# Kernel optimization log

Hardware: AMD Instinct MI355X
Metric: run time of the kernel (lower is better)

The kernel has to match this reference:

```python
import jax, jax.numpy as jnp
import numpy as np

HIDDEN = 1024
HEADS = 16
HEAD_DIM = HIDDEN // HEADS
EPS = 1e-5


def setup_inputs() -> dict:
    key = jax.random.key(0)
    ks = jax.random.split(key, 9)
    B, S, H = 2, 2048, HIDDEN
    scale = 1.0 / np.sqrt(H)
    inp = {
        "hidden_states": jax.random.normal(ks[0], (B, S, H), dtype=jnp.float32),
        "Wq": jax.random.normal(ks[1], (H, H), dtype=jnp.float32) * scale,
        "bq": jnp.zeros((H,), jnp.float32),
        "Wk": jax.random.normal(ks[2], (H, H), dtype=jnp.float32) * scale,
        "bk": jnp.zeros((H,), jnp.float32),
        "Wv": jax.random.normal(ks[3], (H, H), dtype=jnp.float32) * scale,
        "bv": jnp.zeros((H,), jnp.float32),
        "Wo": jax.random.normal(ks[4], (H, H), dtype=jnp.float32) * scale,
        "bo": jnp.zeros((H,), jnp.float32),
        "gamma": jnp.ones((H,), jnp.float32),
        "beta": jnp.zeros((H,), jnp.float32),
    }
    return inp


def reference(hidden_states, Wq, bq, Wk, bk, Wv, bv, Wo, bo, gamma, beta):
    B, S, H = hidden_states.shape
    residual = hidden_states

    def shape(x):  # [B,S,H] -> [B,heads,S,head_dim]
        return x.reshape(B, S, HEADS, HEAD_DIM).transpose(0, 2, 1, 3)

    q = shape(hidden_states @ Wq + bq)
    k = shape(hidden_states @ Wk + bk)
    v = shape(hidden_states @ Wv + bv)

    scores = jnp.einsum("bhqd,bhkd->bhqk", q, k) / jnp.sqrt(
        jnp.asarray(HEAD_DIM, hidden_states.dtype))
    probs = jax.nn.softmax(scores, axis=-1)
    context = jnp.einsum("bhqk,bhkd->bhqd", probs, v)
    context = context.transpose(0, 2, 1, 3).reshape(B, S, H)

    output = context @ Wo + bo
    x = output + residual
    mu = jnp.mean(x, axis=-1, keepdims=True)
    var = jnp.mean(jnp.square(x - mu), axis=-1, keepdims=True)
    return (x - mu) * jax.lax.rsqrt(var + EPS) * gamma + beta
```

## Files before the change

kernel.cpp:

```cpp
#include <hip/hip_runtime.h>
#include <hip/hip_bf16.h>
#include <math.h>

#define HIDDEN 1024
#define HEADS 16
#define HEAD_DIM 64
#define EPS 1e-5f

typedef __attribute__((ext_vector_type(8))) short bf16x8;
typedef __attribute__((ext_vector_type(4))) float f32x4;

#if defined(__has_builtin)
#if __has_builtin(__builtin_amdgcn_exp2f)
#define EXP2(x) __builtin_amdgcn_exp2f(x)
#endif
#endif
#ifndef EXP2
#define EXP2(x) exp2f(x)
#endif

#define QSCALE 0.18033688011112042f

__device__ __forceinline__ short f2bf(float f) {
    union { float f; unsigned u; } v; v.f = f;
    unsigned r = v.u + 0x7fffu + ((v.u >> 16) & 1u);
    return (short)(r >> 16);
}

__device__ __forceinline__ void gl_lds16(const void* g, void* l) {
    __builtin_amdgcn_global_load_lds(
        (const __attribute__((address_space(1))) void*)g,
        (__attribute__((address_space(3))) void*)l, 16, 0, 0);
}

__global__ __launch_bounds__(256) void cast_bf16_kernel(
    const float* __restrict__ in, short* __restrict__ out, int n)
{
    int i = (blockIdx.x * 256 + threadIdx.x) * 4;
    if (i >= n) return;
    float4 v = *(const float4*)(in + i);
    short o[4] = { f2bf(v.x), f2bf(v.y), f2bf(v.z), f2bf(v.w) };
    *(uint2*)(out + i) = *(uint2*)o;
}

__global__ __launch_bounds__(256) void wtrans_kernel(
    const float* __restrict__ Wq, const float* __restrict__ Wk,
    const float* __restrict__ Wv, const float* __restrict__ Wo,
    short* __restrict__ Wt3, short* __restrict__ Wot)
{
    const int wsel = blockIdx.z;
    const float* W = (wsel == 0) ? Wq : (wsel == 1) ? Wk : (wsel == 2) ? Wv : Wo;
    short* dst = (wsel < 3) ? (Wt3 + (size_t)wsel * 1024 * 1024) : Wot;
    const float scale = (wsel == 0) ? QSCALE : 1.0f;

    __shared__ short tile[32][33];
    int n0 = blockIdx.x * 32;
    int k0 = blockIdx.y * 32;
    int tx = threadIdx.x & 31;
    int ty = threadIdx.x >> 5;
    #pragma unroll
    for (int i = 0; i < 32; i += 8)
        tile[ty + i][tx] = f2bf(W[(size_t)(k0 + ty + i) * 1024 + n0 + tx] * scale);
    __syncthreads();
    #pragma unroll
    for (int i = 0; i < 32; i += 8)
        dst[(size_t)(n0 + ty + i) * 1024 + k0 + tx] = tile[tx][ty + i];
}

__global__ __launch_bounds__(256) void concat_bias_kernel(
    const float* __restrict__ bq, const float* __restrict__ bk,
    const float* __restrict__ bv, float* __restrict__ b3)
{
    int i = blockIdx.x * 256 + threadIdx.x;
    if (i >= 3072) return;
    float v = (i < 1024) ? bq[i] * QSCALE
            : (i < 2048) ? bk[i - 1024] : bv[i - 2048];
    b3[i] = v;
}

__global__ __launch_bounds__(256) void gemm_bt_mfma(
    const short* __restrict__ A, const short* __restrict__ Bt,
    const float* __restrict__ bias,
    void* __restrict__ C0, int ldc0,
    void* __restrict__ C1, int split_col, int ldc1,
    const float* __restrict__ resid,
    int M, int N, int K, int out_bf16)
{
    __shared__ short As[128 * 32];
    __shared__ short Bs[128 * 32];
    const int tid = threadIdx.x;
    const int wave = tid >> 6, lane = tid & 63;
    const int ln16 = lane & 15, quad = lane >> 4;
    const int wm = (wave >> 1) * 64, wn = (wave & 1) * 64;
    const int brow = blockIdx.y * 128, bcol = blockIdx.x * 128;

    const int sr  = lane >> 2;
    const int scb = lane & 3;

    f32x4 acc[4][4];
    #pragma unroll
    for (int mt = 0; mt < 4; ++mt)
        #pragma unroll
        for (int nt = 0; nt < 4; ++nt) acc[mt][nt] = (f32x4){0.f, 0.f, 0.f, 0.f};

    for (int k0 = 0; k0 < K; k0 += 32) {
        __syncthreads();
        #pragma unroll
        for (int i = 0; i < 2; ++i) {
            int rb = i * 64 + wave * 16;
            int r  = rb + sr;
            int csrc = (scb ^ ((r >> 1) & 3)) * 8;
            gl_lds16(A  + (size_t)(brow + r) * K + k0 + csrc, &As[rb * 32]);
            gl_lds16(Bt + (size_t)(bcol + r) * K + k0 + csrc, &Bs[rb * 32]);
        }
        __syncthreads();

        bf16x8 af[4], bf[4];
        #pragma unroll
        for (int mt = 0; mt < 4; ++mt) {
            int r = wm + mt * 16 + ln16;
            af[mt] = *(const bf16x8*)&As[r * 32 + ((quad ^ ((r >> 1) & 3)) * 8)];
        }
        #pragma unroll
        for (int nt = 0; nt < 4; ++nt) {
            int r = wn + nt * 16 + ln16;
            bf[nt] = *(const bf16x8*)&Bs[r * 32 + ((quad ^ ((r >> 1) & 3)) * 8)];
        }
        #pragma unroll
        for (int mt = 0; mt < 4; ++mt)
            #pragma unroll
            for (int nt = 0; nt < 4; ++nt)
                acc[mt][nt] = __builtin_amdgcn_mfma_f32_16x16x32_bf16(
                    af[mt], bf[nt], acc[mt][nt], 0, 0, 0);
    }

    void* Cp = C0; int ld = ldc0; int coff = 0;
    if (bcol >= split_col) { Cp = C1; ld = ldc1; coff = split_col; }

    #pragma unroll
    for (int mt = 0; mt < 4; ++mt) {
        #pragma unroll
        for (int r = 0; r < 4; ++r) {
            int row = brow + wm + mt * 16 + quad * 4 + r;
            #pragma unroll
            for (int nt = 0; nt < 4; ++nt) {
                int col = bcol + wn + nt * 16 + ln16;
                float v = acc[mt][nt][r] + bias[col];
                if (resid) v += resid[(size_t)row * N + col];
                if (out_bf16) ((short*)Cp)[(size_t)row * ld + (col - coff)] = f2bf(v);
                else          ((float*)Cp)[(size_t)row * ld + (col - coff)] = v;
            }
        }
    }
}

__global__ __launch_bounds__(256) void vtranspose_kernel(
    const short* __restrict__ Vb, short* __restrict__ VT)
{
    __shared__ short t[64][72];
    const int c0 = blockIdx.x * 64;
    const int r0 = blockIdx.y * 64;
    const int tid = threadIdx.x;
    #pragma unroll
    for (int i = 0; i < 2; ++i) {
        int idx = tid + i * 256;
        int r = idx >> 3, cc = (idx & 7) * 8;
        *(uint4*)&t[r][cc] = *(const uint4*)(Vb + (size_t)(r0 + r) * 1024 + c0 + cc);
    }
    __syncthreads();
    #pragma unroll
    for (int i = 0; i < 2; ++i) {
        int idx = tid + i * 256;
        int c = idx >> 3, rr = (idx & 7) * 8;
        short tmp[8];
        #pragma unroll
        for (int j = 0; j < 8; ++j) tmp[j] = t[rr + j][c];
        *(uint4*)(VT + (size_t)(c0 + c) * 4096 + r0 + rr) = *(uint4*)tmp;
    }
}

__global__ __launch_bounds__(256, 2) void attn_mfma_kernel(
    const short* __restrict__ QKb, const short* __restrict__ VT,
    short* __restrict__ Ctx)
{
    const int S = 2048;
    const int h = blockIdx.x, qt = blockIdx.y, b = blockIdx.z;
    const int tid = threadIdx.x;
    const int wave = tid >> 6, lane = tid & 63;
    const int ln16 = lane & 15, quad = lane >> 4;

    __shared__ alignas(16) char smem[81920];
    char* Pw = smem + 65536 + wave * 4096;

    bf16x8 qf[4][2];
    #pragma unroll
    for (int qg = 0; qg < 4; ++qg)
        #pragma unroll
        for (int kb = 0; kb < 2; ++kb)
            qf[qg][kb] = *(const bf16x8*)(QKb +
                (size_t)(b * S + qt * 64 + qg * 16 + ln16) * 2048 +
                h * 64 + kb * 32 + quad * 8);

    bf16x8 ones;
    #pragma unroll
    for (int j = 0; j < 8; ++j) ones[j] = (short)0x3F80;

    f32x4 of[4][4], lacc[4];
    #pragma unroll
    for (int qg = 0; qg < 4; ++qg) {
        lacc[qg] = (f32x4){0.f, 0.f, 0.f, 0.f};
        #pragma unroll
        for (int nt = 0; nt < 4; ++nt) of[qg][nt] = (f32x4){0.f, 0.f, 0.f, 0.f};
    }

    auto stage = [&](int p, int kt) {
        short* ksb = (short*)(smem + p * 16384);
        short* vsb = (short*)(smem + 32768 + p * 16384);
        const int kr  = lane >> 3;
        const int kb8 = lane & 7;
        const int vr  = lane >> 4;
        const int vb16 = lane & 15;
        #pragma unroll
        for (int i = 0; i < 4; ++i) {
            int r = wave * 32 + i * 8 + kr;
            int ksrc = (kb8 ^ (r & 7)) * 8;
            gl_lds16(QKb + (size_t)(b * S + kt * 128 + r) * 2048 + 1024 + h * 64 + ksrc,
                     ksb + (wave * 32 + i * 8) * 64);
            int d = wave * 16 + i * 4 + vr;
            int vsrc = (vb16 ^ (d & 15)) * 8;
            gl_lds16(VT + (size_t)(h * 64 + d) * 4096 + b * S + kt * 128 + vsrc,
                     vsb + (wave * 16 + i * 4) * 128);
        }
    };

    stage(0, 0);

    for (int kt = 0; kt < 16; ++kt) {
        const int p = kt & 1;

        if (kt + 1 < 16) {
            stage(p ^ 1, kt + 1);
            asm volatile("s_waitcnt vmcnt(8)" ::: "memory");
        } else {
            asm volatile("s_waitcnt vmcnt(0)" ::: "memory");
        }
        __builtin_amdgcn_s_barrier();
        __builtin_amdgcn_sched_barrier(0);

        const short* ks = (const short*)(smem + p * 16384);
        const short* vs = (const short*)(smem + 32768 + p * 16384);
        const int t0w = wave * 32;

        #pragma unroll
        for (int kblk = 0; kblk < 2; ++kblk) {
            int rloc = t0w + kblk * 16 + ln16;
            bf16x8 kf0 = *(const bf16x8*)&ks[rloc * 64 + ((quad ^ (rloc & 7)) * 8)];
            bf16x8 kf1 = *(const bf16x8*)&ks[rloc * 64 + (((4 + quad) ^ (rloc & 7)) * 8)];
            #pragma unroll
            for (int qg = 0; qg < 4; ++qg) {
                f32x4 a = (f32x4){0.f, 0.f, 0.f, 0.f};
                a = __builtin_amdgcn_mfma_f32_16x16x32_bf16(kf0, qf[qg][0], a, 0, 0, 0);
                a = __builtin_amdgcn_mfma_f32_16x16x32_bf16(kf1, qf[qg][1], a, 0, 0, 0);
                float p0 = EXP2(a[0]), p1 = EXP2(a[1]);
                float p2 = EXP2(a[2]), p3 = EXP2(a[3]);
                union { __hip_bfloat162 h2; unsigned u; } c01, c23;
                c01.h2 = __float22bfloat162_rn(make_float2(p0, p1));
                c23.h2 = __float22bfloat162_rn(make_float2(p2, p3));
                uint2 w; w.x = c01.u; w.y = c23.u;
                int qrow = qg * 16 + ln16;
                int key = (qrow >> 1) & 3;
                int bblk = (kblk * 2 + (quad >> 1)) ^ key;
                *(uint2*)(Pw + qrow * 64 + bblk * 16 + (quad & 1) * 8) = w;
            }
        }

        bf16x8 pf[4];
        #pragma unroll
        for (int qg = 0; qg < 4; ++qg) {
            int qrow = qg * 16 + ln16;
            int key = (qrow >> 1) & 3;
            pf[qg] = *(const bf16x8*)(Pw + qrow * 64 + ((quad ^ key) * 16));
            lacc[qg] = __builtin_amdgcn_mfma_f32_16x16x32_bf16(pf[qg], ones, lacc[qg], 0, 0, 0);
        }
        #pragma unroll
        for (int nt = 0; nt < 4; ++nt) {
            int d = nt * 16 + ln16;
            bf16x8 vf = *(const bf16x8*)&vs[d * 128 + (((wave * 4 + quad) ^ (d & 15)) * 8)];
            #pragma unroll
            for (int qg = 0; qg < 4; ++qg)
                of[qg][nt] = __builtin_amdgcn_mfma_f32_16x16x32_bf16(pf[qg], vf, of[qg][nt], 0, 0, 0);
        }

        __builtin_amdgcn_sched_barrier(0);
        __builtin_amdgcn_s_barrier();
    }

    __syncthreads();

    float* Rw = (float*)(smem + wave * 4864);
    float* Lb = (float*)(smem + 4 * 4864);

    if (ln16 == 0) {
        #pragma unroll
        for (int qg = 0; qg < 4; ++qg)
            #pragma unroll
            for (int r = 0; r < 4; ++r)
                Lb[wave * 64 + qg * 16 + quad * 4 + r] = lacc[qg][r];
    }

    const int rq  = tid >> 2;
    const int rd0 = (tid & 3) * 4;
    float inv = 0.f;

    #pragma unroll
    for (int nt = 0; nt < 4; ++nt) {
        #pragma unroll
        for (int qg = 0; qg < 4; ++qg)
            #pragma unroll
            for (int r = 0; r < 4; ++r)
                Rw[(qg * 16 + quad * 4 + r) * 19 + ln16] = of[qg][nt][r];
        __syncthreads();
        if (nt == 0) {
            float l = Lb[rq] + Lb[64 + rq] + Lb[128 + rq] + Lb[192 + rq];
            inv = 1.f / l;
        }
        short o4[4];
        #pragma unroll
        for (int j = 0; j < 4; ++j) {
            int d = rd0 + j;
            float s = 0.f;
            #pragma unroll
            for (int w = 0; w < 4; ++w)
                s += ((const float*)(smem + w * 4864))[rq * 19 + d];
            o4[j] = f2bf(s * inv);
        }
        *(uint2*)(Ctx + (size_t)(b * S + qt * 64 + rq) * 1024 + h * 64 + nt * 16 + rd0) =
            *(uint2*)o4;
        __syncthreads();
    }
}

__global__ __launch_bounds__(256) void resln_kernel(
    const float* __restrict__ xin, const float* __restrict__ gamma,
    const float* __restrict__ beta, float* __restrict__ out)
{
    const int row = blockIdx.x;
    const int tid = threadIdx.x;
    const int wid = tid >> 6, lane = tid & 63;
    __shared__ float red[8];

    float4 x = *(const float4*)(xin + (size_t)row * HIDDEN + tid * 4);
    float s = x.x + x.y + x.z + x.w;
    #pragma unroll
    for (int off = 32; off > 0; off >>= 1) s += __shfl_xor(s, off, 64);
    if (lane == 0) red[wid] = s;
    __syncthreads();
    float mu = (red[0] + red[1] + red[2] + red[3]) * (1.f / HIDDEN);

    float dx = x.x - mu, dy = x.y - mu, dz = x.z - mu, dw = x.w - mu;
    float v = dx * dx + dy * dy + dz * dz + dw * dw;
    #pragma unroll
    for (int off = 32; off > 0; off >>= 1) v += __shfl_xor(v, off, 64);
    if (lane == 0) red[4 + wid] = v;
    __syncthreads();
    float var = (red[4] + red[5] + red[6] + red[7]) * (1.f / HIDDEN);
    float rstd = rsqrtf(var + EPS);

    float4 g = *(const float4*)(gamma + tid * 4);
    float4 bt = *(const float4*)(beta + tid * 4);
    float4 o;
    o.x = dx * rstd * g.x + bt.x;
    o.y = dy * rstd * g.y + bt.y;
    o.z = dz * rstd * g.z + bt.z;
    o.w = dw * rstd * g.w + bt.w;
    *(float4*)(out + (size_t)row * HIDDEN + tid * 4) = o;
}

extern "C" void kernel_launch(void* const* d_in, const int* in_sizes, int n_in,
                              void* d_out, int out_size, void* d_ws, size_t ws_size,
                              hipStream_t stream)
{
    const float* X     = (const float*)d_in[0];
    const float* Wq    = (const float*)d_in[1];
    const float* bq    = (const float*)d_in[2];
    const float* Wk    = (const float*)d_in[3];
    const float* bk    = (const float*)d_in[4];
    const float* Wv    = (const float*)d_in[5];
    const float* bv    = (const float*)d_in[6];
    const float* Wo    = (const float*)d_in[7];
    const float* bo    = (const float*)d_in[8];
    const float* gamma = (const float*)d_in[9];
    const float* beta  = (const float*)d_in[10];
    float* out = (float*)d_out;

    const int B = 2, S = 2048;
    const int M = B * S;
    const size_t mat = (size_t)M * HIDDEN;

    char* ws = (char*)d_ws;
    short* Xb  = (short*)(ws);
    short* VT  = (short*)(ws);
    short* Wot = (short*)(ws + (8ull << 20));
    short* Wt3 = (short*)(ws + (10ull << 20));
    float* b3  = (float*)(ws + (16ull << 20));
    short* QKb = (short*)(ws + (17ull << 20));
    float* Pj  = (float*)(ws + (17ull << 20));
    short* Vb  = (short*)(ws + (33ull << 20));
    short* Ctx = (short*)(ws + (33ull << 20));

    dim3 blk(256);

    cast_bf16_kernel<<<dim3((int)(mat / 4 / 256)), blk, 0, stream>>>(X, Xb, (int)mat);
    wtrans_kernel<<<dim3(32, 32, 4), blk, 0, stream>>>(Wq, Wk, Wv, Wo, Wt3, Wot);
    concat_bias_kernel<<<12, blk, 0, stream>>>(bq, bk, bv, b3);

    dim3 qkvgrid(3072 / 128, M / 128);
    gemm_bt_mfma<<<qkvgrid, blk, 0, stream>>>(Xb, Wt3, b3,
                                              QKb, 2048, Vb, 2048, 1024,
                                              nullptr, M, 3072, HIDDEN, 1);

    vtranspose_kernel<<<dim3(16, 64), blk, 0, stream>>>(Vb, VT);

    dim3 agrid(HEADS, S / 64, B);
    attn_mfma_kernel<<<agrid, blk, 0, stream>>>(QKb, VT, Ctx);

    dim3 ogrid(HIDDEN / 128, M / 128);
    gemm_bt_mfma<<<ogrid, blk, 0, stream>>>(Ctx, Wot, bo,
                                            Pj, 1024, nullptr, 1 << 30, 0,
                                            X, M, HIDDEN, HIDDEN, 0);

    resln_kernel<<<M, blk, 0, stream>>>(Pj, gamma, beta, out);
}
```

Before: 250.6 us.

## Single-buffer attention LDS for higher occupancy, compute row sums in registers, swizzle GEMM tiles

The attention kernel drops K/V double-buffering and overlaps the P scratch with the K/V buffers. This shrinks LDS from 80KB to 32KB so the launch bound can rise to 3 blocks per CU. Row sums of the probabilities are now accumulated in fp32 registers and reduced with shuffles, replacing the extra MFMA against a ones vector. The GEMM remaps block IDs in groups of eight for better L2 locality. In exchange, the attention loop now serialises loading and compute with two full barriers per tile and loses its prefetch overlap, so latency hiding depends on the higher occupancy.

```diff
diff --git a/kernel.cpp b/kernel.cpp
--- a/kernel.cpp
+++ b/kernel.cpp
@@ -92,7 +92,12 @@
     const int wave = tid >> 6, lane = tid & 63;
     const int ln16 = lane & 15, quad = lane >> 4;
     const int wm = (wave >> 1) * 64, wn = (wave & 1) * 64;
-    const int brow = blockIdx.y * 128, bcol = blockIdx.x * 128;
+
+    const int gx = gridDim.x;
+    int bid = blockIdx.y * gx + blockIdx.x;
+    const int cpx = (gx * gridDim.y) >> 3;
+    bid = (bid & 7) * cpx + (bid >> 3);
+    const int brow = (bid / gx) * 128, bcol = (bid % gx) * 128;
 
     const int sr  = lane >> 2;
     const int scb = lane & 3;
@@ -179,7 +184,7 @@
     }
 }
 
-__global__ __launch_bounds__(256, 2) void attn_mfma_kernel(
+__global__ __launch_bounds__(256, 3) void attn_mfma_kernel(
     const short* __restrict__ QKb, const short* __restrict__ VT,
     short* __restrict__ Ctx)
 {
@@ -189,8 +194,10 @@
     const int wave = tid >> 6, lane = tid & 63;
     const int ln16 = lane & 15, quad = lane >> 4;
 
-    __shared__ alignas(16) char smem[81920];
-    char* Pw = smem + 65536 + wave * 4096;
+    __shared__ alignas(16) char smem[32768];
+    short* Ks = (short*)smem;
+    short* Vs = (short*)(smem + 16384);
+    char*  Pw = smem + wave * 4096;
 
     bf16x8 qf[4][2];
     #pragma unroll
@@ -201,21 +208,14 @@
                 (size_t)(b * S + qt * 64 + qg * 16 + ln16) * 2048 +
                 h * 64 + kb * 32 + quad * 8);
 
-    bf16x8 ones;
-    #pragma unroll
-    for (int j = 0; j < 8; ++j) ones[j] = (short)0x3F80;
-
-    f32x4 of[4][4], lacc[4];
-    #pragma unroll
-    for (int qg = 0; qg < 4; ++qg) {
-        lacc[qg] = (f32x4){0.f, 0.f, 0.f, 0.f};
+    f32x4 of[4][4];
+    float rs[4] = {0.f, 0.f, 0.f, 0.f};
+    #pragma unroll
+    for (int qg = 0; qg < 4; ++qg)
         #pragma unroll
         for (int nt = 0; nt < 4; ++nt) of[qg][nt] = (f32x4){0.f, 0.f, 0.f, 0.f};
-    }
-
-    auto stage = [&](int p, int kt) {
-        short* ksb = (short*)(smem + p * 16384);
-        short* vsb = (short*)(smem + 32768 + p * 16384);
+
+    auto stage = [&](int kt) {
         const int kr  = lane >> 3;
         const int kb8 = lane & 7;
         const int vr  = lane >> 4;
@@ -225,44 +225,39 @@
             int r = wave * 32 + i * 8 + kr;
             int ksrc = (kb8 ^ (r & 7)) * 8;
             gl_lds16(QKb + (size_t)(b * S + kt * 128 + r) * 2048 + 1024 + h * 64 + ksrc,
-                     ksb + (wave * 32 + i * 8) * 64);
+                     Ks + (wave * 32 + i * 8) * 64);
             int d = wave * 16 + i * 4 + vr;
             int vsrc = (vb16 ^ (d & 15)) * 8;
             gl_lds16(VT + (size_t)(h * 64 + d) * 4096 + b * S + kt * 128 + vsrc,
-                     vsb + (wave * 16 + i * 4) * 128);
+                     Vs + (wave * 16 + i * 4) * 128);
         }
     };
 
-    stage(0, 0);
-
     for (int kt = 0; kt < 16; ++kt) {
-        const int p = kt & 1;
-
-        if (kt + 1 < 16) {
-            stage(p ^ 1, kt + 1);
-            asm volatile("s_waitcnt vmcnt(8)" ::: "memory");
-        } else {
-            asm volatile("s_waitcnt vmcnt(0)" ::: "memory");
-        }
-        __builtin_amdgcn_s_barrier();
-        __builtin_amdgcn_sched_barrier(0);
-
-        const short* ks = (const short*)(smem + p * 16384);
-        const short* vs = (const short*)(smem + 32768 + p * 16384);
+        if (kt) __syncthreads();
+        stage(kt);
+        __syncthreads();
+
         const int t0w = wave * 32;
 
+        bf16x8 kf[2][2];
         #pragma unroll
         for (int kblk = 0; kblk < 2; ++kblk) {
             int rloc = t0w + kblk * 16 + ln16;
-            bf16x8 kf0 = *(const bf16x8*)&ks[rloc * 64 + ((quad ^ (rloc & 7)) * 8)];
-            bf16x8 kf1 = *(const bf16x8*)&ks[rloc * 64 + (((4 + quad) ^ (rloc & 7)) * 8)];
+            kf[kblk][0] = *(const bf16x8*)&Ks[rloc * 64 + ((quad ^ (rloc & 7)) * 8)];
+            kf[kblk][1] = *(const bf16x8*)&Ks[rloc * 64 + (((4 + quad) ^ (rloc & 7)) * 8)];
+        }
+
+        #pragma unroll
+        for (int kblk = 0; kblk < 2; ++kblk) {
             #pragma unroll
             for (int qg = 0; qg < 4; ++qg) {
                 f32x4 a = (f32x4){0.f, 0.f, 0.f, 0.f};
-                a = __builtin_amdgcn_mfma_f32_16x16x32_bf16(kf0, qf[qg][0], a, 0, 0, 0);
-                a = __builtin_amdgcn_mfma_f32_16x16x32_bf16(kf1, qf[qg][1], a, 0, 0, 0);
+                a = __builtin_amdgcn_mfma_f32_16x16x32_bf16(kf[kblk][0], qf[qg][0], a, 0, 0, 0);
+                a = __builtin_amdgcn_mfma_f32_16x16x32_bf16(kf[kblk][1], qf[qg][1], a, 0, 0, 0);
                 float p0 = EXP2(a[0]), p1 = EXP2(a[1]);
                 float p2 = EXP2(a[2]), p3 = EXP2(a[3]);
+                rs[qg] += (p0 + p1) + (p2 + p3);
                 union { __hip_bfloat162 h2; unsigned u; } c01, c23;
                 c01.h2 = __float22bfloat162_rn(make_float2(p0, p1));
                 c23.h2 = __float22bfloat162_rn(make_float2(p2, p3));
@@ -280,32 +275,32 @@
             int qrow = qg * 16 + ln16;
             int key = (qrow >> 1) & 3;
             pf[qg] = *(const bf16x8*)(Pw + qrow * 64 + ((quad ^ key) * 16));
-            lacc[qg] = __builtin_amdgcn_mfma_f32_16x16x32_bf16(pf[qg], ones, lacc[qg], 0, 0, 0);
         }
         #pragma unroll
         for (int nt = 0; nt < 4; ++nt) {
             int d = nt * 16 + ln16;
-            bf16x8 vf = *(const bf16x8*)&vs[d * 128 + (((wave * 4 + quad) ^ (d & 15)) * 8)];
+            bf16x8 vf = *(const bf16x8*)&Vs[d * 128 + (((wave * 4 + quad) ^ (d & 15)) * 8)];
             #pragma unroll
             for (int qg = 0; qg < 4; ++qg)
                 of[qg][nt] = __builtin_amdgcn_mfma_f32_16x16x32_bf16(pf[qg], vf, of[qg][nt], 0, 0, 0);
         }
-
-        __builtin_amdgcn_sched_barrier(0);
-        __builtin_amdgcn_s_barrier();
     }
 
     __syncthreads();
+
+    #pragma unroll
+    for (int qg = 0; qg < 4; ++qg) {
+        rs[qg] += __shfl_xor(rs[qg], 16, 64);
+        rs[qg] += __shfl_xor(rs[qg], 32, 64);
+    }
 
     float* Rw = (float*)(smem + wave * 4864);
     float* Lb = (float*)(smem + 4 * 4864);
 
-    if (ln16 == 0) {
+    if (quad == 0) {
         #pragma unroll
         for (int qg = 0; qg < 4; ++qg)
-            #pragma unroll
-            for (int r = 0; r < 4; ++r)
-                Lb[wave * 64 + qg * 16 + quad * 4 + r] = lacc[qg][r];
+            Lb[wave * 64 + qg * 16 + ln16] = rs[qg];
     }
 
     const int rq  = tid >> 2;
```

Result: no change. 248.0 us (-1.0%).
